# Optimization experiments

Hardware: AMD Instinct MI355X
Metric: run time of the kernel (lower is better)

The kernel has to match this reference:

```python
import jax, jax.numpy as jnp
import numpy as np

_DIMS = [15, 30, 60, 90, 120, 90, 60, 30, 15, 10, 5, 1]


def setup_inputs() -> dict:
    key = jax.random.key(0)
    keys = jax.random.split(key, 1 + 2 * 11)
    inp = {"x": jax.random.normal(keys[0], (524288, 15), dtype=jnp.float32)}
    for i in range(11):
        fan_in, fan_out = _DIMS[i], _DIMS[i + 1]
        bound = 1.0 / np.sqrt(fan_in)
        inp[f"W{i+1}"] = jax.random.uniform(keys[1 + 2 * i], (fan_out, fan_in), minval=-bound, maxval=bound, dtype=jnp.float32)
        inp[f"b{i+1}"] = jax.random.uniform(keys[2 + 2 * i], (fan_out,), minval=-bound, maxval=bound, dtype=jnp.float32)
    return inp


def reference(x, W1, b1, W2, b2, W3, b3, W4, b4, W5, b5, W6, b6, W7, b7, W8, b8, W9, b9, W10, b10, W11, b11):
    Ws = [W1, W2, W3, W4, W5, W6, W7, W8, W9, W10, W11]
    bs = [b1, b2, b3, b4, b5, b6, b7, b8, b9, b10, b11]
    h = x
    # 10 Linear+ReLU layers, funnel 15->30->60->90->120->90->60->30->15->10->5
    for W, b in zip(Ws[:-1], bs[:-1]):
        h = jax.nn.relu(h @ W.T + b)
    # final Linear 5->1 + sigmoid
    return jax.nn.sigmoid(h @ Ws[-1].T + bs[-1])
```

## Files before the change

kernel.cpp:

```cpp
#include <hip/hip_runtime.h>
#include <math.h>


using bf16x8 = __attribute__((ext_vector_type(8))) short;
using f32x4  = __attribute__((ext_vector_type(4))) float;
using u16x8  = __attribute__((ext_vector_type(8))) unsigned short;
using u32x2  = __attribute__((ext_vector_type(2))) unsigned;
typedef __bf16 bf16x2_t __attribute__((ext_vector_type(2)));

namespace {
constexpr int NL = 11;
constexpr int IN_[NL]   = {15, 30, 60, 90, 120, 90, 60, 30, 15, 10, 5};
constexpr int OUT_[NL]  = {30, 60, 90, 120, 90, 60, 30, 15, 10, 5, 1};
constexpr int KP_[NL]   = {32, 32, 64, 96, 128, 96, 64, 32, 32, 32, 32};
constexpr int NP_[NL]   = {32, 64, 96, 128, 96, 64, 32, 16, 16, 16, 16};
constexpr int WOFF_[NL] = {0, 1024, 3072, 9216, 21504, 33792, 39936, 41984, 42496, 43008, 43520};
constexpr int WTOT      = 44032;
constexpr int ACT_OFF   = WTOT;
constexpr int WAVES     = 8;
constexpr int ROWS_PER_BLOCK = WAVES * 32;
constexpr int ARENA     = 4096;
constexpr int LDS_BYTES = (WTOT + WAVES * ARENA) * 2;
}

__device__ __forceinline__ unsigned short f2bf(float f) {
    unsigned u = __float_as_uint(f);
    u += 0x7fffu + ((u >> 16) & 1u);
    return (unsigned short)(u >> 16);
}

__device__ __forceinline__ unsigned pk2(float a, float b) {
#if __has_builtin(__builtin_amdgcn_cvt_pk_bf16_f32)
    return __builtin_bit_cast(unsigned, __builtin_amdgcn_cvt_pk_bf16_f32(a, b));
#else
    bf16x2_t c;
    c[0] = (__bf16)a;
    c[1] = (__bf16)b;
    return __builtin_bit_cast(unsigned, c);
#endif
}

template <int L>
__device__ __forceinline__ void stage_w(const float* __restrict__ W,
                                        const float* __restrict__ B,
                                        short* wlds, int tid) {
    constexpr int KP = KP_[L], NP = NP_[L], INl = IN_[L], OUTl = OUT_[L];
    constexpr int NKT = KP / 32;
    for (int idx = tid; idx < NP * KP; idx += 512) {
        const int f    = idx >> 9;
        const int t    = idx & 511;
        const int quad = t >> 7;
        const int colc = (t >> 3) & 15;
        const int j    = t & 7;
        const int mt   = f / NKT;
        const int kt   = f - mt * NKT;
        const int m    = mt * 16 + colc;
        const int k    = kt * 32 + quad * 8 + j;
        float v = 0.f;
        if (m < OUTl) {
            if (k < INl) v = W[m * INl + k];
            else if (k == INl) v = B[m];
            else if (k == INl + 1) {
                float hf = __builtin_bit_cast(float, (unsigned)f2bf(B[m]) << 16);
                v = B[m] - hf;
            }
        } else if (m == OUTl || m == OUTl + 1) {
            if (k == INl) v = 1.f;
        }
        wlds[WOFF_[L] + idx] = (short)f2bf(v);
    }
}

template <int L>
__device__ __forceinline__ void layer_fwd(const short* __restrict__ wlds,
                                          short* buf, int col, int quad) {
    constexpr int KP   = KP_[L];
    constexpr int NP   = NP_[L];
    constexpr int NKT  = KP / 32;
    constexpr int NMT  = NP / 16;
    constexpr int KPN  = KP_[L + 1];
    constexpr int NKTN = KPN / 32;
    const short* wl = wlds + WOFF_[L];
    const int fo = quad * 128 + col * 8;

    f32x4 acc[NMT][2];
#pragma unroll
    for (int mt = 0; mt < NMT; ++mt)
#pragma unroll
        for (int b = 0; b < 2; ++b)
            acc[mt][b] = f32x4{0.f, 0.f, 0.f, 0.f};

#pragma unroll
    for (int kt = 0; kt < NKT; ++kt) {
        bf16x8 b0 = *(const bf16x8*)(buf + kt * 512 + fo);
        bf16x8 b1 = *(const bf16x8*)(buf + (NKT + kt) * 512 + fo);
#pragma unroll
        for (int mt = 0; mt < NMT; ++mt) {
            bf16x8 af = *(const bf16x8*)(wl + (mt * NKT + kt) * 512 + fo);
            acc[mt][0] = __builtin_amdgcn_mfma_f32_16x16x32_bf16(af, b0, acc[mt][0], 0, 0, 0);
            acc[mt][1] = __builtin_amdgcn_mfma_f32_16x16x32_bf16(af, b1, acc[mt][1], 0, 0, 0);
        }
    }
#pragma unroll
    for (int mt = 0; mt < NMT; ++mt) {
        const int wbase = (mt >> 1) * 512 + ((mt & 1) * 2 + (quad >> 1)) * 128 + col * 8 + (quad & 1) * 4;
#pragma unroll
        for (int b = 0; b < 2; ++b) {
            u32x2 o;
            o[0] = pk2(fmaxf(acc[mt][b][0], 0.f), fmaxf(acc[mt][b][1], 0.f));
            o[1] = pk2(fmaxf(acc[mt][b][2], 0.f), fmaxf(acc[mt][b][3], 0.f));
            *(u32x2*)(buf + b * NKTN * 512 + wbase) = o;
        }
    }
    if constexpr (NP < KPN) {
        u16x8 z = {0, 0, 0, 0, 0, 0, 0, 0};
        if ((quad & 1) == 0) z[0] = (unsigned short)0x3F80;
        *(u16x8*)(buf + (quad >> 1) * NKTN * 512 + (2 + (quad & 1)) * 128 + col * 8) = z;
    }
}

__device__ __forceinline__ void layer_one(bf16x8 af, short* buf, int col, int quad) {
    const int fo = quad * 128 + col * 8;
    bf16x8 b0 = *(const bf16x8*)(buf + fo);
    bf16x8 b1 = *(const bf16x8*)(buf + 512 + fo);
    f32x4 a0 = f32x4{0.f, 0.f, 0.f, 0.f};
    f32x4 a1 = f32x4{0.f, 0.f, 0.f, 0.f};
    a0 = __builtin_amdgcn_mfma_f32_16x16x32_bf16(af, b0, a0, 0, 0, 0);
    a1 = __builtin_amdgcn_mfma_f32_16x16x32_bf16(af, b1, a1, 0, 0, 0);
    const int wbase = (quad >> 1) * 128 + col * 8 + (quad & 1) * 4;
    u32x2 o0, o1;
    o0[0] = pk2(fmaxf(a0[0], 0.f), fmaxf(a0[1], 0.f));
    o0[1] = pk2(fmaxf(a0[2], 0.f), fmaxf(a0[3], 0.f));
    o1[0] = pk2(fmaxf(a1[0], 0.f), fmaxf(a1[1], 0.f));
    o1[1] = pk2(fmaxf(a1[2], 0.f), fmaxf(a1[3], 0.f));
    *(u32x2*)(buf + wbase) = o0;
    *(u32x2*)(buf + 512 + wbase) = o1;
    u16x8 z = {0, 0, 0, 0, 0, 0, 0, 0};
    if ((quad & 1) == 0) z[0] = (unsigned short)0x3F80;
    *(u16x8*)(buf + (quad >> 1) * 512 + (2 + (quad & 1)) * 128 + col * 8) = z;
}

__device__ __forceinline__ float4 ld4(const float* p) {
    float4 t;
    __builtin_memcpy(&t, p, 16);
    return t;
}

__device__ __forceinline__ void fetch_x(const float* __restrict__ x, int row0,
                                        int col, int quad, float4& a0, float4& a1) {
    const float* r0 = x + (long)(row0 + col) * 15;
    const float* r1 = x + (long)(row0 + 16 + col) * 15;
    if (quad < 3) {
        a0 = ld4(r0 + quad * 4);
        a1 = ld4(r1 + quad * 4);
    } else {
        float4 t0 = ld4(r0 + 11), t1 = ld4(r1 + 11);
        a0 = make_float4(t0.y, t0.z, t0.w, 1.f);
        a1 = make_float4(t1.y, t1.z, t1.w, 1.f);
    }
}

__device__ __forceinline__ void stage_x(short* buf, float4 a0, float4 a1,
                                        int col, int quad) {
    const int off = (quad >> 1) * 128 + col * 8 + (quad & 1) * 4;
    u32x2 o0, o1;
    o0[0] = pk2(a0.x, a0.y); o0[1] = pk2(a0.z, a0.w);
    o1[0] = pk2(a1.x, a1.y); o1[1] = pk2(a1.z, a1.w);
    *(u32x2*)(buf + off) = o0;
    *(u32x2*)(buf + 512 + off) = o1;
    u16x8 z = {0, 0, 0, 0, 0, 0, 0, 0};
    if ((quad & 1) == 0) z[0] = (unsigned short)0x3F80;
    *(u16x8*)(buf + (quad >> 1) * 512 + (2 + (quad & 1)) * 128 + col * 8) = z;
}

extern "C" __global__ void __launch_bounds__(512, 2)
mlp_fused(const float* __restrict__ x,
          const float* __restrict__ W0,  const float* __restrict__ B0,
          const float* __restrict__ W1,  const float* __restrict__ B1,
          const float* __restrict__ W2,  const float* __restrict__ B2,
          const float* __restrict__ W3,  const float* __restrict__ B3,
          const float* __restrict__ W4,  const float* __restrict__ B4,
          const float* __restrict__ W5,  const float* __restrict__ B5,
          const float* __restrict__ W6,  const float* __restrict__ B6,
          const float* __restrict__ W7,  const float* __restrict__ B7,
          const float* __restrict__ W8,  const float* __restrict__ B8,
          const float* __restrict__ W9,  const float* __restrict__ B9,
          const float* __restrict__ W10, const float* __restrict__ B10,
          float* __restrict__ out, int nchunks) {
    extern __shared__ short smem[];
    short* wlds = smem;
    short* act  = smem + ACT_OFF;

    const int tid = threadIdx.x;

    stage_w<0>(W0, B0, wlds, tid);
    stage_w<1>(W1, B1, wlds, tid);
    stage_w<2>(W2, B2, wlds, tid);
    stage_w<3>(W3, B3, wlds, tid);
    stage_w<4>(W4, B4, wlds, tid);
    stage_w<5>(W5, B5, wlds, tid);
    stage_w<6>(W6, B6, wlds, tid);
    stage_w<7>(W7, B7, wlds, tid);
    stage_w<8>(W8, B8, wlds, tid);
    stage_w<9>(W9, B9, wlds, tid);
    stage_w<10>(W10, B10, wlds, tid);
    __syncthreads();

    const int wave = tid >> 6;
    const int lane = tid & 63;
    const int col  = lane & 15;
    const int quad = lane >> 4;
    short* buf = act + wave * ARENA;
    const int fo = quad * 128 + col * 8;

    const bf16x8 w7  = *(const bf16x8*)(wlds + WOFF_[7]  + fo);
    const bf16x8 w8  = *(const bf16x8*)(wlds + WOFF_[8]  + fo);
    const bf16x8 w9  = *(const bf16x8*)(wlds + WOFF_[9]  + fo);
    const bf16x8 w10 = *(const bf16x8*)(wlds + WOFF_[10] + fo);

    int chunk = blockIdx.x;
    float4 xa, xb;
    if (chunk < nchunks)
        fetch_x(x, chunk * ROWS_PER_BLOCK + wave * 32, col, quad, xa, xb);

    for (; chunk < nchunks; chunk += gridDim.x) {
        const int row0 = chunk * ROWS_PER_BLOCK + wave * 32;
        stage_x(buf, xa, xb, col, quad);

        const int nxt = chunk + gridDim.x;
        if (nxt < nchunks)
            fetch_x(x, nxt * ROWS_PER_BLOCK + wave * 32, col, quad, xa, xb);

        layer_fwd<0>(wlds, buf, col, quad);
        layer_fwd<1>(wlds, buf, col, quad);
        layer_fwd<2>(wlds, buf, col, quad);
        layer_fwd<3>(wlds, buf, col, quad);
        layer_fwd<4>(wlds, buf, col, quad);
        layer_fwd<5>(wlds, buf, col, quad);
        layer_fwd<6>(wlds, buf, col, quad);
        layer_one(w7, buf, col, quad);
        layer_one(w8, buf, col, quad);
        layer_one(w9, buf, col, quad);

        {
            bf16x8 b0 = *(const bf16x8*)(buf + fo);
            bf16x8 b1 = *(const bf16x8*)(buf + 512 + fo);
            f32x4 a0 = f32x4{0.f, 0.f, 0.f, 0.f};
            f32x4 a1 = f32x4{0.f, 0.f, 0.f, 0.f};
            a0 = __builtin_amdgcn_mfma_f32_16x16x32_bf16(w10, b0, a0, 0, 0, 0);
            a1 = __builtin_amdgcn_mfma_f32_16x16x32_bf16(w10, b1, a1, 0, 0, 0);
            if (quad == 0) {
                out[row0 + col]      = 1.f / (1.f + __expf(-a0[0]));
                out[row0 + 16 + col] = 1.f / (1.f + __expf(-a1[0]));
            }
        }
    }
}

extern "C" void kernel_launch(void* const* d_in, const int* in_sizes, int n_in,
                              void* d_out, int out_size, void* d_ws, size_t ws_size,
                              hipStream_t stream) {
    (void)n_in; (void)d_ws; (void)ws_size; (void)out_size;
    const float* x = (const float*)d_in[0];
    const float* W[11];
    const float* B[11];
    for (int i = 0; i < 11; ++i) {
        W[i] = (const float*)d_in[1 + 2 * i];
        B[i] = (const float*)d_in[2 + 2 * i];
    }
    const int nrows   = in_sizes[0] / 15;
    const int nchunks = nrows / ROWS_PER_BLOCK;

    hipFuncSetAttribute((const void*)mlp_fused,
                        hipFuncAttributeMaxDynamicSharedMemorySize, LDS_BYTES);

    mlp_fused<<<dim3(256), dim3(512), LDS_BYTES, stream>>>(
        x,
        W[0], B[0], W[1], B[1], W[2], B[2], W[3], B[3], W[4], B[4],
        W[5], B[5], W[6], B[6], W[7], B[7], W[8], B[8], W[9], B[9],
        W[10], B[10],
        (float*)d_out, nchunks);
}
```

Baseline: 200.1 us.

## Process 16 rows per wave with 16 waves per block

Each wave now handles one 16-row tile instead of two, and the block grows from 8 to 16 waves (1024 threads) with a smaller per-wave activation arena. The layer routines, input staging and output store are rewritten for the single-tile layout. The intent is more waves in flight to hide LDS and MFMA latency, and lower register pressure per wave. In exchange, each weight fragment loaded from LDS now feeds only one MFMA instead of two, so LDS weight traffic per row doubles.

```diff
diff --git a/kernel.cpp b/kernel.cpp
--- a/kernel.cpp
+++ b/kernel.cpp
@@ -17,9 +17,11 @@
 constexpr int WOFF_[NL] = {0, 1024, 3072, 9216, 21504, 33792, 39936, 41984, 42496, 43008, 43520};
 constexpr int WTOT      = 44032;
 constexpr int ACT_OFF   = WTOT;
-constexpr int WAVES     = 8;
-constexpr int ROWS_PER_BLOCK = WAVES * 32;
-constexpr int ARENA     = 4096;
+constexpr int WAVES     = 16;
+constexpr int THREADS   = WAVES * 64;
+constexpr int ROWS_PER_WAVE  = 16;
+constexpr int ROWS_PER_BLOCK = WAVES * ROWS_PER_WAVE;
+constexpr int ARENA     = 2048;
 constexpr int LDS_BYTES = (WTOT + WAVES * ARENA) * 2;
 }
 
@@ -46,7 +48,7 @@
                                         short* wlds, int tid) {
     constexpr int KP = KP_[L], NP = NP_[L], INl = IN_[L], OUTl = OUT_[L];
     constexpr int NKT = KP / 32;
-    for (int idx = tid; idx < NP * KP; idx += 512) {
+    for (int idx = tid; idx < NP * KP; idx += THREADS) {
         const int f    = idx >> 9;
         const int t    = idx & 511;
         const int quad = t >> 7;
@@ -79,65 +81,55 @@
     constexpr int NKT  = KP / 32;
     constexpr int NMT  = NP / 16;
     constexpr int KPN  = KP_[L + 1];
-    constexpr int NKTN = KPN / 32;
     const short* wl = wlds + WOFF_[L];
     const int fo = quad * 128 + col * 8;
 
-    f32x4 acc[NMT][2];
+    f32x4 acc[NMT];
 #pragma unroll
     for (int mt = 0; mt < NMT; ++mt)
-#pragma unroll
-        for (int b = 0; b < 2; ++b)
-            acc[mt][b] = f32x4{0.f, 0.f, 0.f, 0.f};
+        acc[mt] = f32x4{0.f, 0.f, 0.f, 0.f};
 
 #pragma unroll
     for (int kt = 0; kt < NKT; ++kt) {
         bf16x8 b0 = *(const bf16x8*)(buf + kt * 512 + fo);
-        bf16x8 b1 = *(const bf16x8*)(buf + (NKT + kt) * 512 + fo);
 #pragma unroll
         for (int mt = 0; mt < NMT; ++mt) {
             bf16x8 af = *(const bf16x8*)(wl + (mt * NKT + kt) * 512 + fo);
-            acc[mt][0] = __builtin_amdgcn_mfma_f32_16x16x32_bf16(af, b0, acc[mt][0], 0, 0, 0);
-            acc[mt][1] = __builtin_amdgcn_mfma_f32_16x16x32_bf16(af, b1, acc[mt][1], 0, 0, 0);
+            acc[mt] = __builtin_amdgcn_mfma_f32_16x16x32_bf16(af, b0, acc[mt], 0, 0, 0);
         }
     }
 #pragma unroll
     for (int mt = 0; mt < NMT; ++mt) {
         const int wbase = (mt >> 1) * 512 + ((mt & 1) * 2 + (quad >> 1)) * 128 + col * 8 + (quad & 1) * 4;
-#pragma unroll
-        for (int b = 0; b < 2; ++b) {
-            u32x2 o;
-            o[0] = pk2(fmaxf(acc[mt][b][0], 0.f), fmaxf(acc[mt][b][1], 0.f));
-            o[1] = pk2(fmaxf(acc[mt][b][2], 0.f), fmaxf(acc[mt][b][3], 0.f));
-            *(u32x2*)(buf + b * NKTN * 512 + wbase) = o;
-        }
+        u32x2 o;
+        o[0] = pk2(fmaxf(acc[mt][0], 0.f), fmaxf(acc[mt][1], 0.f));
+        o[1] = pk2(fmaxf(acc[mt][2], 0.f), fmaxf(acc[mt][3], 0.f));
+        *(u32x2*)(buf + wbase) = o;
     }
     if constexpr (NP < KPN) {
-        u16x8 z = {0, 0, 0, 0, 0, 0, 0, 0};
-        if ((quad & 1) == 0) z[0] = (unsigned short)0x3F80;
-        *(u16x8*)(buf + (quad >> 1) * NKTN * 512 + (2 + (quad & 1)) * 128 + col * 8) = z;
+        if (quad < 2) {
+            u16x8 z = {0, 0, 0, 0, 0, 0, 0, 0};
+            if (quad == 0) z[0] = (unsigned short)0x3F80;
+            *(u16x8*)(buf + (2 + quad) * 128 + col * 8) = z;
+        }
     }
 }
 
 __device__ __forceinline__ void layer_one(bf16x8 af, short* buf, int col, int quad) {
     const int fo = quad * 128 + col * 8;
     bf16x8 b0 = *(const bf16x8*)(buf + fo);
-    bf16x8 b1 = *(const bf16x8*)(buf + 512 + fo);
     f32x4 a0 = f32x4{0.f, 0.f, 0.f, 0.f};
-    f32x4 a1 = f32x4{0.f, 0.f, 0.f, 0.f};
     a0 = __builtin_amdgcn_mfma_f32_16x16x32_bf16(af, b0, a0, 0, 0, 0);
-    a1 = __builtin_amdgcn_mfma_f32_16x16x32_bf16(af, b1, a1, 0, 0, 0);
     const int wbase = (quad >> 1) * 128 + col * 8 + (quad & 1) * 4;
-    u32x2 o0, o1;
+    u32x2 o0;
     o0[0] = pk2(fmaxf(a0[0], 0.f), fmaxf(a0[1], 0.f));
     o0[1] = pk2(fmaxf(a0[2], 0.f), fmaxf(a0[3], 0.f));
-    o1[0] = pk2(fmaxf(a1[0], 0.f), fmaxf(a1[1], 0.f));
-    o1[1] = pk2(fmaxf(a1[2], 0.f), fmaxf(a1[3], 0.f));
     *(u32x2*)(buf + wbase) = o0;
-    *(u32x2*)(buf + 512 + wbase) = o1;
-    u16x8 z = {0, 0, 0, 0, 0, 0, 0, 0};
-    if ((quad & 1) == 0) z[0] = (unsigned short)0x3F80;
-    *(u16x8*)(buf + (quad >> 1) * 512 + (2 + (quad & 1)) * 128 + col * 8) = z;
+    if (quad < 2) {
+        u16x8 z = {0, 0, 0, 0, 0, 0, 0, 0};
+        if (quad == 0) z[0] = (unsigned short)0x3F80;
+        *(u16x8*)(buf + (2 + quad) * 128 + col * 8) = z;
+    }
 }
 
 __device__ __forceinline__ float4 ld4(const float* p) {
@@ -147,33 +139,29 @@
 }
 
 __device__ __forceinline__ void fetch_x(const float* __restrict__ x, int row0,
-                                        int col, int quad, float4& a0, float4& a1) {
+                                        int col, int quad, float4& a0) {
     const float* r0 = x + (long)(row0 + col) * 15;
-    const float* r1 = x + (long)(row0 + 16 + col) * 15;
     if (quad < 3) {
         a0 = ld4(r0 + quad * 4);
-        a1 = ld4(r1 + quad * 4);
     } else {
-        float4 t0 = ld4(r0 + 11), t1 = ld4(r1 + 11);
+        float4 t0 = ld4(r0 + 11);
         a0 = make_float4(t0.y, t0.z, t0.w, 1.f);
-        a1 = make_float4(t1.y, t1.z, t1.w, 1.f);
-    }
-}
-
-__device__ __forceinline__ void stage_x(short* buf, float4 a0, float4 a1,
-                                        int col, int quad) {
+    }
+}
+
+__device__ __forceinline__ void stage_x(short* buf, float4 a0, int col, int quad) {
     const int off = (quad >> 1) * 128 + col * 8 + (quad & 1) * 4;
-    u32x2 o0, o1;
+    u32x2 o0;
     o0[0] = pk2(a0.x, a0.y); o0[1] = pk2(a0.z, a0.w);
-    o1[0] = pk2(a1.x, a1.y); o1[1] = pk2(a1.z, a1.w);
     *(u32x2*)(buf + off) = o0;
-    *(u32x2*)(buf + 512 + off) = o1;
-    u16x8 z = {0, 0, 0, 0, 0, 0, 0, 0};
-    if ((quad & 1) == 0) z[0] = (unsigned short)0x3F80;
-    *(u16x8*)(buf + (quad >> 1) * 512 + (2 + (quad & 1)) * 128 + col * 8) = z;
-}
-
-extern "C" __global__ void __launch_bounds__(512, 2)
+    if (quad < 2) {
+        u16x8 z = {0, 0, 0, 0, 0, 0, 0, 0};
+        if (quad == 0) z[0] = (unsigned short)0x3F80;
+        *(u16x8*)(buf + (2 + quad) * 128 + col * 8) = z;
+    }
+}
+
+extern "C" __global__ void __launch_bounds__(THREADS, 4)
 mlp_fused(const float* __restrict__ x,
           const float* __restrict__ W0,  const float* __restrict__ B0,
           const float* __restrict__ W1,  const float* __restrict__ B1,
@@ -219,17 +207,17 @@
     const bf16x8 w10 = *(const bf16x8*)(wlds + WOFF_[10] + fo);
 
     int chunk = blockIdx.x;
-    float4 xa, xb;
+    float4 xa;
     if (chunk < nchunks)
-        fetch_x(x, chunk * ROWS_PER_BLOCK + wave * 32, col, quad, xa, xb);
+        fetch_x(x, chunk * ROWS_PER_BLOCK + wave * ROWS_PER_WAVE, col, quad, xa);
 
     for (; chunk < nchunks; chunk += gridDim.x) {
-        const int row0 = chunk * ROWS_PER_BLOCK + wave * 32;
-        stage_x(buf, xa, xb, col, quad);
+        const int row0 = chunk * ROWS_PER_BLOCK + wave * ROWS_PER_WAVE;
+        stage_x(buf, xa, col, quad);
 
         const int nxt = chunk + gridDim.x;
         if (nxt < nchunks)
-            fetch_x(x, nxt * ROWS_PER_BLOCK + wave * 32, col, quad, xa, xb);
+            fetch_x(x, nxt * ROWS_PER_BLOCK + wave * ROWS_PER_WAVE, col, quad, xa);
 
         layer_fwd<0>(wlds, buf, col, quad);
         layer_fwd<1>(wlds, buf, col, quad);
@@ -244,15 +232,10 @@
 
         {
             bf16x8 b0 = *(const bf16x8*)(buf + fo);
-            bf16x8 b1 = *(const bf16x8*)(buf + 512 + fo);
             f32x4 a0 = f32x4{0.f, 0.f, 0.f, 0.f};
-            f32x4 a1 = f32x4{0.f, 0.f, 0.f, 0.f};
             a0 = __builtin_amdgcn_mfma_f32_16x16x32_bf16(w10, b0, a0, 0, 0, 0);
-            a1 = __builtin_amdgcn_mfma_f32_16x16x32_bf16(w10, b1, a1, 0, 0, 0);
-            if (quad == 0) {
-                out[row0 + col]      = 1.f / (1.f + __expf(-a0[0]));
-                out[row0 + 16 + col] = 1.f / (1.f + __expf(-a1[0]));
-            }
+            if (quad == 0)
+                out[row0 + col] = 1.f / (1.f + __expf(-a0[0]));
         }
     }
 }
@@ -274,7 +257,7 @@
     hipFuncSetAttribute((const void*)mlp_fused,
                         hipFuncAttributeMaxDynamicSharedMemorySize, LDS_BYTES);
 
-    mlp_fused<<<dim3(256), dim3(512), LDS_BYTES, stream>>>(
+    mlp_fused<<<dim3(256), dim3(THREADS), LDS_BYTES, stream>>>(
         x,
         W[0], B[0], W[1], B[1], W[2], B[2], W[3], B[3], W[4], B[4],
         W[5], B[5], W[6], B[6], W[7], B[7], W[8], B[8], W[9], B[9],
```

Measured after the change: 182.9 us. 1.09x faster.

## Keep layer-2 and tail weights in registers, shrink LDS, use 10 waves

Applied to the files above, without the earlier changes.

Layer 2's weight fragments (12 bf16x8) and the tail-layer weights are staged temporarily in the activation arena, loaded into registers, and then that space is reused, so the persistent weight region in LDS shrinks. With the saved LDS the block grows to 10 waves (640 threads) and launch bounds ask for 3 blocks per CU. The per-layer constant-one padding writes are removed: each wave's arena is zeroed once and only the bias lane is written. Rows are bounds-checked for a partial last chunk. This raises register pressure and changes rows per block, which could cause spills or load imbalance across the fixed 256-block grid.

```diff
diff --git a/kernel.cpp b/kernel.cpp
--- a/kernel.cpp
+++ b/kernel.cpp
@@ -14,12 +14,23 @@
 constexpr int OUT_[NL]  = {30, 60, 90, 120, 90, 60, 30, 15, 10, 5, 1};
 constexpr int KP_[NL]   = {32, 32, 64, 96, 128, 96, 64, 32, 32, 32, 32};
 constexpr int NP_[NL]   = {32, 64, 96, 128, 96, 64, 32, 16, 16, 16, 16};
-constexpr int WOFF_[NL] = {0, 1024, 3072, 9216, 21504, 33792, 39936, 41984, 42496, 43008, 43520};
-constexpr int WTOT      = 44032;
-constexpr int ACT_OFF   = WTOT;
-constexpr int WAVES     = 8;
-constexpr int ROWS_PER_BLOCK = WAVES * 32;
-constexpr int ARENA     = 4096;
+constexpr int WP0 = 0;
+constexpr int WP1 = 1024;
+constexpr int WP3 = 3072;
+constexpr int WP4 = 15360;
+constexpr int WP5 = 27648;
+constexpr int WP6 = 33792;
+constexpr int WTOT = 35840;
+constexpr int T2  = 0;
+constexpr int T7  = 6144;
+constexpr int T8  = 6656;
+constexpr int T9  = 7168;
+constexpr int T10 = 7680;
+constexpr int WAVES   = 10;
+constexpr int THREADS = WAVES * 64;
+constexpr int ROWS_PER_WAVE  = 32;
+constexpr int ROWS_PER_BLOCK = WAVES * ROWS_PER_WAVE;
+constexpr int ARENA   = 4096;
 constexpr int LDS_BYTES = (WTOT + WAVES * ARENA) * 2;
 }
 
@@ -43,10 +54,10 @@
 template <int L>
 __device__ __forceinline__ void stage_w(const float* __restrict__ W,
                                         const float* __restrict__ B,
-                                        short* wlds, int tid) {
+                                        short* dst, int tid) {
     constexpr int KP = KP_[L], NP = NP_[L], INl = IN_[L], OUTl = OUT_[L];
     constexpr int NKT = KP / 32;
-    for (int idx = tid; idx < NP * KP; idx += 512) {
+    for (int idx = tid; idx < NP * KP; idx += THREADS) {
         const int f    = idx >> 9;
         const int t    = idx & 511;
         const int quad = t >> 7;
@@ -67,20 +78,18 @@
         } else if (m == OUTl || m == OUTl + 1) {
             if (k == INl) v = 1.f;
         }
-        wlds[WOFF_[L] + idx] = (short)f2bf(v);
+        dst[idx] = (short)f2bf(v);
     }
 }
 
 template <int L>
-__device__ __forceinline__ void layer_fwd(const short* __restrict__ wlds,
+__device__ __forceinline__ void layer_fwd(const short* __restrict__ wl,
                                           short* buf, int col, int quad) {
     constexpr int KP   = KP_[L];
     constexpr int NP   = NP_[L];
     constexpr int NKT  = KP / 32;
     constexpr int NMT  = NP / 16;
-    constexpr int KPN  = KP_[L + 1];
-    constexpr int NKTN = KPN / 32;
-    const short* wl = wlds + WOFF_[L];
+    constexpr int NKTN = KP_[L + 1] / 32;
     const int fo = quad * 128 + col * 8;
 
     f32x4 acc[NMT][2];
@@ -112,10 +121,38 @@
             *(u32x2*)(buf + b * NKTN * 512 + wbase) = o;
         }
     }
-    if constexpr (NP < KPN) {
-        u16x8 z = {0, 0, 0, 0, 0, 0, 0, 0};
-        if ((quad & 1) == 0) z[0] = (unsigned short)0x3F80;
-        *(u16x8*)(buf + (quad >> 1) * NKTN * 512 + (2 + (quad & 1)) * 128 + col * 8) = z;
+}
+
+__device__ __forceinline__ void layer2_pre(const bf16x8 (&wf)[12],
+                                           short* buf, int col, int quad) {
+    constexpr int NKT = 2, NMT = 6, NKTN = 3;
+    const int fo = quad * 128 + col * 8;
+    f32x4 acc[NMT][2];
+#pragma unroll
+    for (int mt = 0; mt < NMT; ++mt)
+#pragma unroll
+        for (int b = 0; b < 2; ++b)
+            acc[mt][b] = f32x4{0.f, 0.f, 0.f, 0.f};
+#pragma unroll
+    for (int kt = 0; kt < NKT; ++kt) {
+        bf16x8 b0 = *(const bf16x8*)(buf + kt * 512 + fo);
+        bf16x8 b1 = *(const bf16x8*)(buf + (NKT + kt) * 512 + fo);
+#pragma unroll
+        for (int mt = 0; mt < NMT; ++mt) {
+            acc[mt][0] = __builtin_amdgcn_mfma_f32_16x16x32_bf16(wf[mt * NKT + kt], b0, acc[mt][0], 0, 0, 0);
+            acc[mt][1] = __builtin_amdgcn_mfma_f32_16x16x32_bf16(wf[mt * NKT + kt], b1, acc[mt][1], 0, 0, 0);
+        }
+    }
+#pragma unroll
+    for (int mt = 0; mt < NMT; ++mt) {
+        const int wbase = (mt >> 1) * 512 + ((mt & 1) * 2 + (quad >> 1)) * 128 + col * 8 + (quad & 1) * 4;
+#pragma unroll
+        for (int b = 0; b < 2; ++b) {
+            u32x2 o;
+            o[0] = pk2(fmaxf(acc[mt][b][0], 0.f), fmaxf(acc[mt][b][1], 0.f));
+            o[1] = pk2(fmaxf(acc[mt][b][2], 0.f), fmaxf(acc[mt][b][3], 0.f));
+            *(u32x2*)(buf + b * NKTN * 512 + wbase) = o;
+        }
     }
 }
 
@@ -135,9 +172,10 @@
     o1[1] = pk2(fmaxf(a1[2], 0.f), fmaxf(a1[3], 0.f));
     *(u32x2*)(buf + wbase) = o0;
     *(u32x2*)(buf + 512 + wbase) = o1;
-    u16x8 z = {0, 0, 0, 0, 0, 0, 0, 0};
-    if ((quad & 1) == 0) z[0] = (unsigned short)0x3F80;
-    *(u16x8*)(buf + (quad >> 1) * 512 + (2 + (quad & 1)) * 128 + col * 8) = z;
+    if (quad == 0) {
+        buf[256 + col * 8]       = (short)0x3F80;
+        buf[512 + 256 + col * 8] = (short)0x3F80;
+    }
 }
 
 __device__ __forceinline__ float4 ld4(const float* p) {
@@ -147,14 +185,17 @@
 }
 
 __device__ __forceinline__ void fetch_x(const float* __restrict__ x, int row0,
-                                        int col, int quad, float4& a0, float4& a1) {
-    const float* r0 = x + (long)(row0 + col) * 15;
-    const float* r1 = x + (long)(row0 + 16 + col) * 15;
+                                        int nrows, int col, int quad,
+                                        float4& a0, float4& a1) {
+    int r0 = row0 + col;      if (r0 > nrows - 1) r0 = nrows - 1;
+    int r1 = row0 + 16 + col; if (r1 > nrows - 1) r1 = nrows - 1;
+    const float* p0 = x + (long)r0 * 15;
+    const float* p1 = x + (long)r1 * 15;
     if (quad < 3) {
-        a0 = ld4(r0 + quad * 4);
-        a1 = ld4(r1 + quad * 4);
+        a0 = ld4(p0 + quad * 4);
+        a1 = ld4(p1 + quad * 4);
     } else {
-        float4 t0 = ld4(r0 + 11), t1 = ld4(r1 + 11);
+        float4 t0 = ld4(p0 + 11), t1 = ld4(p1 + 11);
         a0 = make_float4(t0.y, t0.z, t0.w, 1.f);
         a1 = make_float4(t1.y, t1.z, t1.w, 1.f);
     }
@@ -168,12 +209,13 @@
     o1[0] = pk2(a1.x, a1.y); o1[1] = pk2(a1.z, a1.w);
     *(u32x2*)(buf + off) = o0;
     *(u32x2*)(buf + 512 + off) = o1;
-    u16x8 z = {0, 0, 0, 0, 0, 0, 0, 0};
-    if ((quad & 1) == 0) z[0] = (unsigned short)0x3F80;
-    *(u16x8*)(buf + (quad >> 1) * 512 + (2 + (quad & 1)) * 128 + col * 8) = z;
-}
-
-extern "C" __global__ void __launch_bounds__(512, 2)
+    if (quad == 0) {
+        buf[256 + col * 8]       = (short)0x3F80;
+        buf[512 + 256 + col * 8] = (short)0x3F80;
+    }
+}
+
+extern "C" __global__ void __launch_bounds__(THREADS, 3)
 mlp_fused(const float* __restrict__ x,
           const float* __restrict__ W0,  const float* __restrict__ B0,
           const float* __restrict__ W1,  const float* __restrict__ B1,
@@ -186,24 +228,24 @@
           const float* __restrict__ W8,  const float* __restrict__ B8,
           const float* __restrict__ W9,  const float* __restrict__ B9,
           const float* __restrict__ W10, const float* __restrict__ B10,
-          float* __restrict__ out, int nchunks) {
+          float* __restrict__ out, int nchunks, int nrows) {
     extern __shared__ short smem[];
     short* wlds = smem;
-    short* act  = smem + ACT_OFF;
+    short* act  = smem + WTOT;
 
     const int tid = threadIdx.x;
 
-    stage_w<0>(W0, B0, wlds, tid);
-    stage_w<1>(W1, B1, wlds, tid);
-    stage_w<2>(W2, B2, wlds, tid);
-    stage_w<3>(W3, B3, wlds, tid);
-    stage_w<4>(W4, B4, wlds, tid);
-    stage_w<5>(W5, B5, wlds, tid);
-    stage_w<6>(W6, B6, wlds, tid);
-    stage_w<7>(W7, B7, wlds, tid);
-    stage_w<8>(W8, B8, wlds, tid);
-    stage_w<9>(W9, B9, wlds, tid);
-    stage_w<10>(W10, B10, wlds, tid);
+    stage_w<0>(W0, B0, wlds + WP0, tid);
+    stage_w<1>(W1, B1, wlds + WP1, tid);
+    stage_w<3>(W3, B3, wlds + WP3, tid);
+    stage_w<4>(W4, B4, wlds + WP4, tid);
+    stage_w<5>(W5, B5, wlds + WP5, tid);
+    stage_w<6>(W6, B6, wlds + WP6, tid);
+    stage_w<2>(W2, B2, act + T2, tid);
+    stage_w<7>(W7, B7, act + T7, tid);
+    stage_w<8>(W8, B8, act + T8, tid);
+    stage_w<9>(W9, B9, act + T9, tid);
+    stage_w<10>(W10, B10, act + T10, tid);
     __syncthreads();
 
     const int wave = tid >> 6;
@@ -213,31 +255,43 @@
     short* buf = act + wave * ARENA;
     const int fo = quad * 128 + col * 8;
 
-    const bf16x8 w7  = *(const bf16x8*)(wlds + WOFF_[7]  + fo);
-    const bf16x8 w8  = *(const bf16x8*)(wlds + WOFF_[8]  + fo);
-    const bf16x8 w9  = *(const bf16x8*)(wlds + WOFF_[9]  + fo);
-    const bf16x8 w10 = *(const bf16x8*)(wlds + WOFF_[10] + fo);
+    bf16x8 wf2[12];
+#pragma unroll
+    for (int i = 0; i < 12; ++i)
+        wf2[i] = *(const bf16x8*)(act + T2 + i * 512 + fo);
+    const bf16x8 w7  = *(const bf16x8*)(act + T7  + fo);
+    const bf16x8 w8  = *(const bf16x8*)(act + T8  + fo);
+    const bf16x8 w9  = *(const bf16x8*)(act + T9  + fo);
+    const bf16x8 w10 = *(const bf16x8*)(act + T10 + fo);
+    __syncthreads();
+
+    {
+        u16x8 z = {0, 0, 0, 0, 0, 0, 0, 0};
+#pragma unroll
+        for (int i = 0; i < 8; ++i)
+            *(u16x8*)(buf + (lane + i * 64) * 8) = z;
+    }
 
     int chunk = blockIdx.x;
     float4 xa, xb;
     if (chunk < nchunks)
-        fetch_x(x, chunk * ROWS_PER_BLOCK + wave * 32, col, quad, xa, xb);
+        fetch_x(x, chunk * ROWS_PER_BLOCK + wave * ROWS_PER_WAVE, nrows, col, quad, xa, xb);
 
     for (; chunk < nchunks; chunk += gridDim.x) {
-        const int row0 = chunk * ROWS_PER_BLOCK + wave * 32;
+        const int row0 = chunk * ROWS_PER_BLOCK + wave * ROWS_PER_WAVE;
         stage_x(buf, xa, xb, col, quad);
 
         const int nxt = chunk + gridDim.x;
         if (nxt < nchunks)
-            fetch_x(x, nxt * ROWS_PER_BLOCK + wave * 32, col, quad, xa, xb);
-
-        layer_fwd<0>(wlds, buf, col, quad);
-        layer_fwd<1>(wlds, buf, col, quad);
-        layer_fwd<2>(wlds, buf, col, quad);
-        layer_fwd<3>(wlds, buf, col, quad);
-        layer_fwd<4>(wlds, buf, col, quad);
-        layer_fwd<5>(wlds, buf, col, quad);
-        layer_fwd<6>(wlds, buf, col, quad);
+            fetch_x(x, nxt * ROWS_PER_BLOCK + wave * ROWS_PER_WAVE, nrows, col, quad, xa, xb);
+
+        layer_fwd<0>(wlds + WP0, buf, col, quad);
+        layer_fwd<1>(wlds + WP1, buf, col, quad);
+        layer2_pre(wf2, buf, col, quad);
+        layer_fwd<3>(wlds + WP3, buf, col, quad);
+        layer_fwd<4>(wlds + WP4, buf, col, quad);
+        layer_fwd<5>(wlds + WP5, buf, col, quad);
+        layer_fwd<6>(wlds + WP6, buf, col, quad);
         layer_one(w7, buf, col, quad);
         layer_one(w8, buf, col, quad);
         layer_one(w9, buf, col, quad);
@@ -250,8 +304,10 @@
             a0 = __builtin_amdgcn_mfma_f32_16x16x32_bf16(w10, b0, a0, 0, 0, 0);
             a1 = __builtin_amdgcn_mfma_f32_16x16x32_bf16(w10, b1, a1, 0, 0, 0);
             if (quad == 0) {
-                out[row0 + col]      = 1.f / (1.f + __expf(-a0[0]));
-                out[row0 + 16 + col] = 1.f / (1.f + __expf(-a1[0]));
+                const int r0 = row0 + col;
+                const int r1 = row0 + 16 + col;
+                if (r0 < nrows) out[r0] = 1.f / (1.f + __expf(-a0[0]));
+                if (r1 < nrows) out[r1] = 1.f / (1.f + __expf(-a1[0]));
             }
         }
     }
@@ -269,15 +325,15 @@
         B[i] = (const float*)d_in[2 + 2 * i];
     }
     const int nrows   = in_sizes[0] / 15;
-    const int nchunks = nrows / ROWS_PER_BLOCK;
+    const int nchunks = (nrows + ROWS_PER_BLOCK - 1) / ROWS_PER_BLOCK;
 
     hipFuncSetAttribute((const void*)mlp_fused,
                         hipFuncAttributeMaxDynamicSharedMemorySize, LDS_BYTES);
 
-    mlp_fused<<<dim3(256), dim3(512), LDS_BYTES, stream>>>(
+    mlp_fused<<<dim3(256), dim3(THREADS), LDS_BYTES, stream>>>(
         x,
         W[0], B[0], W[1], B[1], W[2], B[2], W[3], B[3], W[4], B[4],
         W[5], B[5], W[6], B[6], W[7], B[7], W[8], B[8], W[9], B[9],
         W[10], B[10],
-        (float*)d_out, nchunks);
-}
+        (float*)d_out, nchunks, nrows);
+}
```

After: 200.4 us. Within noise of the previous version (+0.1%).
